# Performance work log

Measured on AMD Instinct MI355X. Metric: run time of the kernel, lower is better.

Reference implementation:

```python
import jax, jax.numpy as jnp
import numpy as np
import math

D, H, L, FF, V = 512, 8, 6, 2048, 512
DK = D // H
EPS = 1e-5


def _pos_encoding(seq_len, d_model):
    pos = np.arange(seq_len, dtype=np.float32)[:, None]
    div = np.exp(np.arange(0, d_model, 2, dtype=np.float32) * (-math.log(10000.0) / d_model))
    pe = np.zeros((seq_len, d_model), dtype=np.float32)
    pe[:, 0::2] = np.sin(pos * div)
    pe[:, 1::2] = np.cos(pos * div)
    return jnp.asarray(pe)


def _layernorm(x, g, b):
    mu = jnp.mean(x, axis=-1, keepdims=True)
    var = jnp.mean(jnp.square(x - mu), axis=-1, keepdims=True)
    return (x - mu) * jax.lax.rsqrt(var + EPS) * g + b


def setup_inputs() -> dict:
    key = jax.random.key(0)
    ks = jax.random.split(key, 16)
    B, S = 4, 1024
    inp = {
        'input_ids': jax.random.randint(ks[0], (B, S), 0, V, dtype=jnp.int64),
        'attention_mask': jnp.ones((B, S), dtype=jnp.int32),
        'emb': 0.02 * jax.random.normal(ks[1], (V, D), jnp.float32),
        # per-layer stacked params, torch Linear layout [out, in]
        'wq': 0.02 * jax.random.normal(ks[2], (L, D, D), jnp.float32),
        'bq': jnp.zeros((L, D), jnp.float32),
        'wk': 0.02 * jax.random.normal(ks[3], (L, D, D), jnp.float32),
        'bk': jnp.zeros((L, D), jnp.float32),
        'wv': 0.02 * jax.random.normal(ks[4], (L, D, D), jnp.float32),
        'bv': jnp.zeros((L, D), jnp.float32),
        'wo': 0.02 * jax.random.normal(ks[5], (L, D, D), jnp.float32),
        'bo': jnp.zeros((L, D), jnp.float32),
        'ln1_g': jnp.ones((L, D), jnp.float32),
        'ln1_b': jnp.zeros((L, D), jnp.float32),
        'w1': 0.02 * jax.random.normal(ks[6], (L, FF, D), jnp.float32),
        'b1': jnp.zeros((L, FF), jnp.float32),
        'w2': 0.02 * jax.random.normal(ks[7], (L, D, FF), jnp.float32),
        'b2': jnp.zeros((L, D), jnp.float32),
        'ln2_g': jnp.ones((L, D), jnp.float32),
        'ln2_b': jnp.zeros((L, D), jnp.float32),
        'lnf_g': jnp.ones((D,), jnp.float32),
        'lnf_b': jnp.zeros((D,), jnp.float32),
        'lm_w': 0.02 * jax.random.normal(ks[8], (V, D), jnp.float32),
    }
    return inp


def reference(input_ids, attention_mask, emb, wq, bq, wk, bk, wv, bv, wo, bo,
              ln1_g, ln1_b, w1, b1, w2, b2, ln2_g, ln2_b, lnf_g, lnf_b, lm_w):
    B, S = input_ids.shape
    x = emb[input_ids] * math.sqrt(D) + _pos_encoding(S, D)[None]  # [B,S,D]
    causal = jnp.tril(jnp.ones((S, S), jnp.float32))
    mask = causal[None, None] * attention_mask[:, None, None, :].astype(jnp.float32)  # [B,1,S,S]

    def step(h, p):
        (lwq, lbq, lwk, lbk, lwv, lbv, lwo, lbo, g1, be1, lw1, lb1, lw2, lb2, g2, be2) = p
        q = (jnp.einsum('bsd,ed->bse', h, lwq) + lbq).reshape(B, S, H, DK).transpose(0, 2, 1, 3)
        k = (jnp.einsum('bsd,ed->bse', h, lwk) + lbk).reshape(B, S, H, DK).transpose(0, 2, 1, 3)
        v = (jnp.einsum('bsd,ed->bse', h, lwv) + lbv).reshape(B, S, H, DK).transpose(0, 2, 1, 3)
        scores = jnp.einsum('bhqd,bhkd->bhqk', q, k) / math.sqrt(DK)
        scores = jnp.where(mask == 0, jnp.float32(-1e9), scores)
        attn = jax.nn.softmax(scores, axis=-1)
        o = jnp.einsum('bhqk,bhkd->bhqd', attn, v).transpose(0, 2, 1, 3).reshape(B, S, D)
        o = jnp.einsum('bsd,ed->bse', o, lwo) + lbo
        h = _layernorm(h + o, g1, be1)
        f = jax.nn.relu(jnp.einsum('bsd,fd->bsf', h, lw1) + lb1)
        f = jnp.einsum('bsf,df->bsd', f, lw2) + lb2
        h = _layernorm(h + f, g2, be2)
        return h, None

    x, _ = jax.lax.scan(step, x, (wq, bq, wk, bk, wv, bv, wo, bo,
                                  ln1_g, ln1_b, w1, b1, w2, b2, ln2_g, ln2_b))
    x = _layernorm(x, lnf_g, lnf_b)
    logits = jnp.einsum('bsd,vd->bsv', x, lm_w)  # [B,S,V]
    return logits
```

## Files before the change

### kernel.cpp

```cpp
#include <hip/hip_runtime.h>
#include <math.h>

#define D_MODEL 512
#define NHEAD   8
#define DKH     64
#define NLAYER  6
#define FFDIM   2048
#define VOCAB   512
#define BB      4
#define SS      1024
#define NROWS   4096

typedef unsigned short ushort_t;
typedef short short8 __attribute__((ext_vector_type(8)));
typedef float f32x4  __attribute__((ext_vector_type(4)));

__device__ __forceinline__ float bf2f(ushort_t u) {
    union { float f; unsigned int i; } x; x.i = ((unsigned int)u) << 16; return x.f;
}
__device__ __forceinline__ ushort_t f2bf(float f) {
    union { float f; unsigned int i; } x; x.f = f;
    unsigned int r = x.i + 0x7FFFu + ((x.i >> 16) & 1u);
    return (ushort_t)(r >> 16);
}
__device__ __forceinline__ void gload_lds16(const void* g, void* l) {
    __builtin_amdgcn_global_load_lds(
        (const __attribute__((address_space(1))) void*)g,
        (__attribute__((address_space(3))) void*)l, 16, 0, 0);
}
__device__ __forceinline__ void block_barrier() {
    __builtin_amdgcn_s_barrier();
    __builtin_amdgcn_sched_barrier(0);
}

__global__ __launch_bounds__(256) void cvt_all(
    const float* __restrict__ wq, const float* __restrict__ wk, const float* __restrict__ wv,
    const float* __restrict__ wo, const float* __restrict__ w1, const float* __restrict__ w2,
    const float* __restrict__ bq, const float* __restrict__ bk, const float* __restrict__ bv,
    ushort_t* __restrict__ wl, float* __restrict__ bqkv,
    const float* __restrict__ lmw, ushort_t* __restrict__ lmwb,
    const int* __restrict__ am, float* __restrict__ mbias)
{
    const int bidx = blockIdx.x;
    const int tt = threadIdx.x;
    if (bidx < 18432) {
        int idx = bidx * 256 + tt;
        int e = idx * 4;
        int l = e / 3145728;
        int off = e - l * 3145728;
        float4 v;
        if (off < 786432) {
            if (off < 262144)       v = *(const float4*)(wq + l * 262144 + off);
            else if (off < 524288)  v = *(const float4*)(wk + l * 262144 + (off - 262144));
            else                    v = *(const float4*)(wv + l * 262144 + (off - 524288));
        } else if (off < 1048576)   v = *(const float4*)(wo + l * 262144 + (off - 786432));
        else if (off < 2097152)     v = *(const float4*)(w1 + l * 1048576 + (off - 1048576));
        else                        v = *(const float4*)(w2 + l * 1048576 + (off - 2097152));
        union { ushort_t u[4]; uint2 q; } pk;
        pk.u[0] = f2bf(v.x); pk.u[1] = f2bf(v.y); pk.u[2] = f2bf(v.z); pk.u[3] = f2bf(v.w);
        *(uint2*)(wl + e) = pk.q;
        if (idx < 2304) {
            int b4 = idx * 4;
            int bl = b4 / 1536;
            int r  = b4 - bl * 1536;
            float4 bv4;
            if (r < 512)       bv4 = *(const float4*)(bq + bl * 512 + r);
            else if (r < 1024) bv4 = *(const float4*)(bk + bl * 512 + (r - 512));
            else               bv4 = *(const float4*)(bv + bl * 512 + (r - 1024));
            *(float4*)(bqkv + b4) = bv4;
        }
    } else if (bidx < 18688) {
        int e = ((bidx - 18432) * 256 + tt) * 4;
        float4 v = *(const float4*)(lmw + e);
        union { ushort_t u[4]; uint2 q; } pk;
        pk.u[0] = f2bf(v.x); pk.u[1] = f2bf(v.y); pk.u[2] = f2bf(v.z); pk.u[3] = f2bf(v.w);
        *(uint2*)(lmwb + e) = pk.q;
    } else {
#pragma unroll
        for (int i = 0; i < 16; ++i) {
            int j = i * 256 + tt;
            mbias[j] = am[j] ? 0.f : -1e9f;
        }
    }
}

__global__ __launch_bounds__(256) void cvt_layer(
    const float* __restrict__ wq, const float* __restrict__ wk, const float* __restrict__ wv,
    const float* __restrict__ wo, const float* __restrict__ w1, const float* __restrict__ w2,
    const float* __restrict__ bq, const float* __restrict__ bk, const float* __restrict__ bv,
    ushort_t* __restrict__ wl, float* __restrict__ bqkv)
{
    int idx = blockIdx.x * 256 + threadIdx.x;
    int e = idx * 4;
    float4 v;
    if (e < 786432) {
        if (e < 262144)       v = *(const float4*)(wq + e);
        else if (e < 524288)  v = *(const float4*)(wk + (e - 262144));
        else                  v = *(const float4*)(wv + (e - 524288));
    } else if (e < 1048576)   v = *(const float4*)(wo + (e - 786432));
    else if (e < 2097152)     v = *(const float4*)(w1 + (e - 1048576));
    else                      v = *(const float4*)(w2 + (e - 2097152));
    union { ushort_t u[4]; uint2 q; } pk;
    pk.u[0] = f2bf(v.x); pk.u[1] = f2bf(v.y); pk.u[2] = f2bf(v.z); pk.u[3] = f2bf(v.w);
    *(uint2*)(wl + e) = pk.q;
    if (idx < 384) {
        int b4 = idx * 4;
        float4 bv4;
        if (b4 < 512)       bv4 = *(const float4*)(bq + b4);
        else if (b4 < 1024) bv4 = *(const float4*)(bk + (b4 - 512));
        else                bv4 = *(const float4*)(bv + (b4 - 1024));
        *(float4*)(bqkv + b4) = bv4;
    }
}

__global__ __launch_bounds__(256) void cvt_simple(
    const float* __restrict__ src, ushort_t* __restrict__ dst)
{
    int e = (blockIdx.x * 256 + threadIdx.x) * 4;
    float4 v = *(const float4*)(src + e);
    union { ushort_t u[4]; uint2 q; } pk;
    pk.u[0] = f2bf(v.x); pk.u[1] = f2bf(v.y); pk.u[2] = f2bf(v.z); pk.u[3] = f2bf(v.w);
    *(uint2*)(dst + e) = pk.q;
}

__global__ __launch_bounds__(256) void maskbias_kernel(
    const int* __restrict__ am, float* __restrict__ mb)
{
    int i = blockIdx.x * 256 + threadIdx.x;
    if (i < NROWS) mb[i] = am[i] ? 0.f : -1e9f;
}

__global__ __launch_bounds__(512) void embed_kernel(
    const int* __restrict__ ids, const float* __restrict__ emb,
    float* __restrict__ xf, ushort_t* __restrict__ xb)
{
    int row = blockIdx.x;
    int d   = threadIdx.x;
    int s   = row & (SS - 1);
    int tok = ids[row];
    float div = expf(-(float)(d & ~1) * 0.0179889460390586f);
    float arg = (float)s * div;
    float pe  = (d & 1) ? cosf(arg) : sinf(arg);
    float v = emb[(size_t)tok * D_MODEL + d] * 22.62741699796952f + pe;
    xf[(size_t)row * D_MODEL + d] = v;
    xb[(size_t)row * D_MODEL + d] = f2bf(v);
}

__global__ __launch_bounds__(512) void ln_kernel(
    const float* __restrict__ x, const float* __restrict__ g,
    const float* __restrict__ b, float* __restrict__ outf, ushort_t* __restrict__ outb)
{
    int row = blockIdx.x;
    int d   = threadIdx.x;
    int wave = d >> 6, lane = d & 63;
    __shared__ float red[8];

    float v = x[(size_t)row * D_MODEL + d];
    float s = v;
#pragma unroll
    for (int o = 32; o > 0; o >>= 1) s += __shfl_xor(s, o);
    if (lane == 0) red[wave] = s;
    __syncthreads();
    float tot = 0.f;
#pragma unroll
    for (int i = 0; i < 8; ++i) tot += red[i];
    float mu = tot * (1.0f / D_MODEL);
    float c  = v - mu;
    __syncthreads();
    float s2 = c * c;
#pragma unroll
    for (int o = 32; o > 0; o >>= 1) s2 += __shfl_xor(s2, o);
    if (lane == 0) red[wave] = s2;
    __syncthreads();
    float tot2 = 0.f;
#pragma unroll
    for (int i = 0; i < 8; ++i) tot2 += red[i];
    float var = tot2 * (1.0f / D_MODEL);
    float y = c * (1.0f / sqrtf(var + 1e-5f)) * g[d] + b[d];
    outf[(size_t)row * D_MODEL + d] = y;
    outb[(size_t)row * D_MODEL + d] = f2bf(y);
}

template<int BM, int BN, bool RELU, bool RES, bool OBF16, bool VT>
__global__ __launch_bounds__(256) void gemm_kernel(
    const ushort_t* __restrict__ A, const ushort_t* __restrict__ W,
    const float* __restrict__ bias, const float* __restrict__ res,
    void* __restrict__ out, ushort_t* __restrict__ vtg, int M, int N, int K)
{
    constexpr int WMT = BM / 2, WNT = BN / 2;
    constexpr int FM = WMT / 16, FN = WNT / 16;
    constexpr int ISSA = BM / 32, ISSB = BN / 32;
    __shared__ ushort_t As[BM * 64];
    __shared__ ushort_t Bs[BN * 64];

    const int t = threadIdx.x;
    const int w = t >> 6, lane = t & 63;
    const int wr = w >> 1, wc = w & 1;
    const int col0 = blockIdx.x * BN;
    const int row0 = blockIdx.y * BM;
    const int lrow = lane & 15, kg = lane >> 4;
    const int srow = t >> 3;
    const int sk8  = (t & 7) ^ ((t >> 3) & 7);

    f32x4 acc[FM][FN];
#pragma unroll
    for (int m = 0; m < FM; ++m)
#pragma unroll
        for (int n = 0; n < FN; ++n) acc[m][n] = (f32x4){0.f, 0.f, 0.f, 0.f};

    for (int k0 = 0; k0 < K; k0 += 64) {
#pragma unroll
        for (int i = 0; i < ISSA; ++i)
            gload_lds16(A + (size_t)(row0 + i * 32 + srow) * K + k0 + sk8 * 8,
                        (char*)As + i * 4096 + t * 16);
#pragma unroll
        for (int i = 0; i < ISSB; ++i)
            gload_lds16(W + (size_t)(col0 + i * 32 + srow) * K + k0 + sk8 * 8,
                        (char*)Bs + i * 4096 + t * 16);
        __syncthreads();
#pragma unroll
        for (int kk = 0; kk < 2; ++kk) {
            short8 af[FM], bfv[FN];
#pragma unroll
            for (int m = 0; m < FM; ++m) {
                const int row = wr * WMT + m * 16 + lrow;
                af[m] = *(const short8*)&As[row * 64 + (((kk * 4 + kg) ^ (lrow & 7)) << 3)];
            }
#pragma unroll
            for (int n = 0; n < FN; ++n) {
                const int col = wc * WNT + n * 16 + lrow;
                bfv[n] = *(const short8*)&Bs[col * 64 + (((kk * 4 + kg) ^ (lrow & 7)) << 3)];
            }
#pragma unroll
            for (int m = 0; m < FM; ++m)
#pragma unroll
                for (int n = 0; n < FN; ++n)
                    acc[m][n] = __builtin_amdgcn_mfma_f32_16x16x32_bf16(
                        af[m], bfv[n], acc[m][n], 0, 0, 0);
        }
        __syncthreads();
    }

    const int lrow4 = (lane >> 4) * 4;
    const int lcol  = lane & 15;
#pragma unroll
    for (int m = 0; m < FM; ++m)
#pragma unroll
        for (int n = 0; n < FN; ++n) {
            const int col = col0 + wc * WNT + n * 16 + lcol;
            const float bv = bias ? bias[col] : 0.f;
            const int row_base = row0 + wr * WMT + m * 16 + lrow4;
            if (VT && col >= 1024) {
                const int vh = (col - 1024) >> 6;
                const int vd = (col - 1024) & 63;
                const int bq = row_base >> 10;
                const int s0 = row_base & 1023;
                union { ushort_t u[4]; uint2 q; } pk;
#pragma unroll
                for (int j = 0; j < 4; ++j) pk.u[j] = f2bf(acc[m][n][j] + bv);
                *(uint2*)(vtg + ((size_t)(bq * 8 + vh) * 64 + vd) * 1024 + s0) = pk.q;
            } else {
#pragma unroll
                for (int j = 0; j < 4; ++j) {
                    const int row = row_base + j;
                    float v = acc[m][n][j] + bv;
                    if (RES)  v += res[(size_t)row * N + col];
                    if (RELU) v = fmaxf(v, 0.f);
                    if (OBF16) ((ushort_t*)out)[(size_t)row * N + col] = f2bf(v);
                    else       ((float*)out)[(size_t)row * N + col] = v;
                }
            }
        }
}

__global__ __launch_bounds__(256) void attn_kernel(
    const ushort_t* __restrict__ qkv, const ushort_t* __restrict__ vtg,
    const float* __restrict__ mbias, ushort_t* __restrict__ o)
{
    __shared__ ushort_t Kl[3][64 * 64];
    __shared__ ushort_t Vl[3][64 * 64];

    const int t = threadIdx.x, w = t >> 6, l = t & 63;
    const int bid = blockIdx.x;
    const int qt = 15 - (bid >> 5);
    const int bh = bid & 31, b = bh >> 3, h = bh & 7;
    const int q0 = qt * 64;
    const int lg = l >> 4, lr = l & 15;
    const int qi = q0 + w * 16 + lr;

    const ushort_t* qrow = qkv + (size_t)(b * SS + qi) * 1536 + h * 64;
    const short8 qa0 = *(const short8*)(qrow + lg * 8);
    const short8 qa1 = *(const short8*)(qrow + 32 + lg * 8);

    float m_run = -1e30f, l_run = 0.f;
    f32x4 oacc[4];
#pragma unroll
    for (int nb = 0; nb < 4; ++nb) oacc[nb] = (f32x4){0.f, 0.f, 0.f, 0.f};

    const int krow = 32 * ((lr >> 1) & 1) + 8 * (lr >> 2) + (lr & 1);
    const ushort_t* qkvK = qkv + (size_t)(b * SS) * 1536 + 512 + h * 64;
    const ushort_t* vtgB = vtg + (size_t)bh * 64 * 1024;
    const float*    mb0  = mbias + b * SS + 8 * lg;

    const int sr0 = t >> 3, sc0 = t & 7;

    auto STAGE = [&](int buf, int kt) {
#pragma unroll
        for (int p = 0; p < 2; ++p) {
            const int row = p * 32 + sr0;
            const int ch  = sc0 ^ ((row >> 3) & 7);
            gload_lds16(qkvK + (size_t)(kt * 64 + row) * 1536 + ch * 8,
                        (char*)&Kl[buf][0] + (p * 256 + t) * 16);
        }
#pragma unroll
        for (int p = 0; p < 2; ++p) {
            const int row = p * 32 + sr0;
            const int ch  = sc0 ^ (row & 7);
            gload_lds16(vtgB + (size_t)row * 1024 + kt * 64 + ch * 8,
                        (char*)&Vl[buf][0] + (p * 256 + t) * 16);
        }
    };

    auto COMPUTE = [&](int buf, int kt) {
        const ushort_t* Kb = &Kl[buf][0];
        const ushort_t* Vb = &Vl[buf][0];
        short8 kf[8], vf[8];
#pragma unroll
        for (int nf = 0; nf < 4; ++nf) {
            const int row = 2 * nf + krow;
            const int sw  = (row >> 3) & 7;
            kf[2 * nf]     = *(const short8*)&Kb[row * 64 + ((lg ^ sw) << 3)];
            kf[2 * nf + 1] = *(const short8*)&Kb[row * 64 + (((4 + lg) ^ sw) << 3)];
        }
#pragma unroll
        for (int nb = 0; nb < 4; ++nb) {
            const int row = 16 * nb + lr;
            const int sw  = row & 7;
            vf[2 * nb]     = *(const short8*)&Vb[row * 64 + ((lg ^ sw) << 3)];
            vf[2 * nb + 1] = *(const short8*)&Vb[row * 64 + (((4 + lg) ^ sw) << 3)];
        }
        const float* mrow = mb0 + kt * 64;
        const float4 mA = *(const float4*)(mrow);
        const float4 mB = *(const float4*)(mrow + 4);
        const float4 mC = *(const float4*)(mrow + 32);
        const float4 mD = *(const float4*)(mrow + 36);
        f32x4 s[4];
#pragma unroll
        for (int nf = 0; nf < 4; ++nf) {
            f32x4 a = (f32x4){0.f, 0.f, 0.f, 0.f};
            a = __builtin_amdgcn_mfma_f32_16x16x32_bf16(kf[2 * nf],     qa0, a, 0, 0, 0);
            a = __builtin_amdgcn_mfma_f32_16x16x32_bf16(kf[2 * nf + 1], qa1, a, 0, 0, 0);
            s[nf] = a;
        }
        const bool diag = (kt == qt);
        const int kbase = kt * 64 + 8 * lg;
#pragma unroll
        for (int nf = 0; nf < 4; ++nf) {
#pragma unroll
            for (int r = 0; r < 4; ++r) {
                const int e = r & 1, oo = (r >> 1) & 1;
                const int idx = 2 * nf + e;
                const float bias = oo ? (idx < 4 ? ((const float*)&mC)[idx] : ((const float*)&mD)[idx - 4])
                                      : (idx < 4 ? ((const float*)&mA)[idx] : ((const float*)&mB)[idx - 4]);
                float sv = s[nf][r] * 0.125f + bias;
                if (diag && (kbase + idx + 32 * oo) > qi) sv = -1e9f;
                s[nf][r] = sv;
            }
        }
        float pm[4];
#pragma unroll
        for (int nf = 0; nf < 4; ++nf)
            pm[nf] = fmaxf(fmaxf(s[nf][0], s[nf][1]), fmaxf(s[nf][2], s[nf][3]));
        float mx = fmaxf(fmaxf(pm[0], pm[1]), fmaxf(pm[2], pm[3]));
        mx = fmaxf(mx, __shfl_xor(mx, 16));
        mx = fmaxf(mx, __shfl_xor(mx, 32));
        const float mnew = fmaxf(m_run, mx);
        const float rs   = __expf(m_run - mnew);
        m_run = mnew;
        float ps[4];
#pragma unroll
        for (int nf = 0; nf < 4; ++nf) {
#pragma unroll
            for (int r = 0; r < 4; ++r) s[nf][r] = __expf(s[nf][r] - mnew);
            ps[nf] = (s[nf][0] + s[nf][1]) + (s[nf][2] + s[nf][3]);
        }
        float tsum = (ps[0] + ps[1]) + (ps[2] + ps[3]);
        tsum += __shfl_xor(tsum, 16);
        tsum += __shfl_xor(tsum, 32);
        l_run = l_run * rs + tsum;
#pragma unroll
        for (int nb = 0; nb < 4; ++nb)
#pragma unroll
            for (int r = 0; r < 4; ++r) oacc[nb][r] *= rs;
        union { unsigned u[4]; short8 s8; } pa0u, pa1u;
#pragma unroll
        for (int nf = 0; nf < 4; ++nf) {
            pa0u.u[nf] = ((unsigned)f2bf(s[nf][1]) << 16) | (unsigned)f2bf(s[nf][0]);
            pa1u.u[nf] = ((unsigned)f2bf(s[nf][3]) << 16) | (unsigned)f2bf(s[nf][2]);
        }
#pragma unroll
        for (int nb = 0; nb < 4; ++nb) {
            oacc[nb] = __builtin_amdgcn_mfma_f32_16x16x32_bf16(vf[2 * nb],     pa0u.s8, oacc[nb], 0, 0, 0);
            oacc[nb] = __builtin_amdgcn_mfma_f32_16x16x32_bf16(vf[2 * nb + 1], pa1u.s8, oacc[nb], 0, 0, 0);
        }
    };

    STAGE(0, 0);
    if (qt >= 1) STAGE(1, 1);
    int buf = 0;
    for (int kt = 0; kt <= qt; ++kt) {
        if (kt + 2 <= qt) {
            int nxt = buf + 2; if (nxt >= 3) nxt -= 3;
            STAGE(nxt, kt + 2);
            asm volatile("s_waitcnt vmcnt(8)" ::: "memory");
        } else if (kt + 1 <= qt) {
            asm volatile("s_waitcnt vmcnt(4)" ::: "memory");
        } else {
            asm volatile("s_waitcnt vmcnt(0)" ::: "memory");
        }
        block_barrier();
        COMPUTE(buf, kt);
        block_barrier();
        if (++buf == 3) buf = 0;
    }

    const float inv = 1.0f / l_run;
    ushort_t* orow = o + (size_t)(b * SS + qi) * 512 + h * 64;
#pragma unroll
    for (int nb = 0; nb < 4; ++nb) {
        union { ushort_t u[4]; uint2 q; } pk;
#pragma unroll
        for (int r = 0; r < 4; ++r) pk.u[r] = f2bf(oacc[nb][r] * inv);
        *(uint2*)(orow + nb * 16 + 4 * lg) = pk.q;
    }
}

extern "C" void kernel_launch(void* const* d_in, const int* in_sizes, int n_in,
                              void* d_out, int out_size, void* d_ws, size_t ws_size,
                              hipStream_t stream)
{
    const int*   ids   = (const int*)d_in[0];
    const int*   am    = (const int*)d_in[1];
    const float* emb   = (const float*)d_in[2];
    const float* wq    = (const float*)d_in[3];
    const float* bq    = (const float*)d_in[4];
    const float* wk    = (const float*)d_in[5];
    const float* bk    = (const float*)d_in[6];
    const float* wv    = (const float*)d_in[7];
    const float* bv    = (const float*)d_in[8];
    const float* wo    = (const float*)d_in[9];
    const float* bo    = (const float*)d_in[10];
    const float* ln1g  = (const float*)d_in[11];
    const float* ln1b  = (const float*)d_in[12];
    const float* w1    = (const float*)d_in[13];
    const float* b1    = (const float*)d_in[14];
    const float* w2    = (const float*)d_in[15];
    const float* b2    = (const float*)d_in[16];
    const float* ln2g  = (const float*)d_in[17];
    const float* ln2b  = (const float*)d_in[18];
    const float* lnfg  = (const float*)d_in[19];
    const float* lnfb  = (const float*)d_in[20];
    const float* lmw   = (const float*)d_in[21];

    char* base = (char*)d_ws;
    float*    h    = (float*)(base);
    float*    h2   = (float*)(base + 8388608);
    ushort_t* hb   = (ushort_t*)(base + 16777216);
    ushort_t* act  = (ushort_t*)(base + 20971520);
    ushort_t* qkvb = act;
    ushort_t* ob   = act + 6291456;
    ushort_t* fbuf = act;
    ushort_t* vtg  = (ushort_t*)h2;

    const bool onep = ws_size >= (size_t)76100000;
    ushort_t* wl   = (ushort_t*)(base + 37748736);
    float*    bqkv; ushort_t* lmwb; float* mbias;
    if (onep) {
        bqkv  = (float*)(base + 75497472);
        lmwb  = (ushort_t*)(base + 75534336);
        mbias = (float*)(base + 76058624);
    } else {
        bqkv  = (float*)(base + 44040192);
        lmwb  = (ushort_t*)(base + 44046336);
        mbias = (float*)(base + 44570624);
    }

    embed_kernel<<<NROWS, 512, 0, stream>>>(ids, emb, h, hb);
    if (onep) {
        cvt_all<<<18689, 256, 0, stream>>>(wq, wk, wv, wo, w1, w2, bq, bk, bv,
                                           wl, bqkv, lmw, lmwb, am, mbias);
    } else {
        cvt_simple<<<256, 256, 0, stream>>>(lmw, lmwb);
        maskbias_kernel<<<16, 256, 0, stream>>>(am, mbias);
    }

    for (int l = 0; l < NLAYER; ++l) {
        const size_t dd = (size_t)l * 262144;
        const size_t fd = (size_t)l * 1048576;
        ushort_t* lw; const float* lb;
        if (onep) {
            lw = wl + (size_t)l * 3145728;
            lb = bqkv + l * 1536;
        } else {
            cvt_layer<<<3072, 256, 0, stream>>>(wq + dd, wk + dd, wv + dd, wo + dd,
                                                w1 + fd, w2 + fd,
                                                bq + l * 512, bk + l * 512, bv + l * 512,
                                                wl, bqkv);
            lw = wl;
            lb = bqkv;
        }
        gemm_kernel<64, 128, false, false, true, true><<<dim3(12, 64), 256, 0, stream>>>(
            hb, lw, lb, nullptr, qkvb, vtg, NROWS, 1536, 512);

        attn_kernel<<<512, 256, 0, stream>>>(qkvb, vtg, mbias, ob);

        gemm_kernel<64, 64, false, true, false, false><<<dim3(8, 64), 256, 0, stream>>>(
            ob, lw + 786432, bo + l * 512, h, h2, nullptr, NROWS, 512, 512);
        ln_kernel<<<NROWS, 512, 0, stream>>>(h2, ln1g + l * 512, ln1b + l * 512, h, hb);

        gemm_kernel<64, 128, true, false, true, false><<<dim3(16, 64), 256, 0, stream>>>(
            hb, lw + 1048576, b1 + l * 2048, nullptr, fbuf, nullptr, NROWS, 2048, 512);
        gemm_kernel<64, 64, false, true, false, false><<<dim3(8, 64), 256, 0, stream>>>(
            fbuf, lw + 2097152, b2 + l * 512, h, h2, nullptr, NROWS, 512, 2048);
        ln_kernel<<<NROWS, 512, 0, stream>>>(h2, ln2g + l * 512, ln2b + l * 512, h, hb);
    }

    ln_kernel<<<NROWS, 512, 0, stream>>>(h, lnfg, lnfb, h, hb);
    gemm_kernel<64, 64, false, false, false, false><<<dim3(8, 64), 256, 0, stream>>>(
        hb, lmwb, nullptr, nullptr, d_out, nullptr, NROWS, 512, 512);
}
```

Baseline: 704.8 us.

## Add multi-stage LDS prefetch pipeline with explicit vmcnt waits to GEMM

Adds a DEPTH template parameter to the GEMM so global-to-LDS loads for upcoming K tiles are issued before computing the current tile, with double or triple buffering chosen per call site. Synchronisation uses explicit s_waitcnt vmcnt counts plus raw barriers instead of __syncthreads. The goal is to overlap memory latency with MFMA work. In exchange it uses more shared memory, which may lower occupancy, and it relies on the vmcnt counts matching the number of loads each stage issues.

```diff
diff --git a/kernel.cpp b/kernel.cpp
--- a/kernel.cpp
+++ b/kernel.cpp
@@ -27,6 +27,13 @@
     __builtin_amdgcn_global_load_lds(
         (const __attribute__((address_space(1))) void*)g,
         (__attribute__((address_space(3))) void*)l, 16, 0, 0);
+}
+template<int N> __device__ __forceinline__ void waitcnt_vm() {
+    if constexpr (N == 0)      asm volatile("s_waitcnt vmcnt(0)" ::: "memory");
+    else if constexpr (N == 4) asm volatile("s_waitcnt vmcnt(4)" ::: "memory");
+    else if constexpr (N == 6) asm volatile("s_waitcnt vmcnt(6)" ::: "memory");
+    else if constexpr (N == 8) asm volatile("s_waitcnt vmcnt(8)" ::: "memory");
+    else if constexpr (N == 12) asm volatile("s_waitcnt vmcnt(12)" ::: "memory");
 }
 __device__ __forceinline__ void block_barrier() {
     __builtin_amdgcn_s_barrier();
@@ -181,7 +188,7 @@
     outb[(size_t)row * D_MODEL + d] = f2bf(y);
 }
 
-template<int BM, int BN, bool RELU, bool RES, bool OBF16, bool VT>
+template<int BM, int BN, int DEPTH, bool RELU, bool RES, bool OBF16, bool VT>
 __global__ __launch_bounds__(256) void gemm_kernel(
     const ushort_t* __restrict__ A, const ushort_t* __restrict__ W,
     const float* __restrict__ bias, const float* __restrict__ res,
@@ -190,8 +197,9 @@
     constexpr int WMT = BM / 2, WNT = BN / 2;
     constexpr int FM = WMT / 16, FN = WNT / 16;
     constexpr int ISSA = BM / 32, ISSB = BN / 32;
-    __shared__ ushort_t As[BM * 64];
-    __shared__ ushort_t Bs[BN * 64];
+    constexpr int NL = ISSA + ISSB;
+    __shared__ ushort_t As[DEPTH][BM * 64];
+    __shared__ ushort_t Bs[DEPTH][BN * 64];
 
     const int t = threadIdx.x;
     const int w = t >> 6, lane = t & 63;
@@ -208,28 +216,50 @@
 #pragma unroll
         for (int n = 0; n < FN; ++n) acc[m][n] = (f32x4){0.f, 0.f, 0.f, 0.f};
 
-    for (int k0 = 0; k0 < K; k0 += 64) {
+    auto STAGE = [&](int sb, int k0) {
 #pragma unroll
         for (int i = 0; i < ISSA; ++i)
             gload_lds16(A + (size_t)(row0 + i * 32 + srow) * K + k0 + sk8 * 8,
-                        (char*)As + i * 4096 + t * 16);
+                        (char*)&As[sb][0] + i * 4096 + t * 16);
 #pragma unroll
         for (int i = 0; i < ISSB; ++i)
             gload_lds16(W + (size_t)(col0 + i * 32 + srow) * K + k0 + sk8 * 8,
-                        (char*)Bs + i * 4096 + t * 16);
-        __syncthreads();
+                        (char*)&Bs[sb][0] + i * 4096 + t * 16);
+    };
+
+    const int NIT = K >> 6;
+    STAGE(0, 0);
+    if constexpr (DEPTH >= 3) { if (NIT > 1) STAGE(1, 64); }
+
+    int buf = 0;
+    for (int it = 0; it < NIT; ++it) {
+        if constexpr (DEPTH == 1) {
+            if (it > 0) STAGE(0, it * 64);
+            waitcnt_vm<0>();
+        } else if constexpr (DEPTH == 2) {
+            if (it + 1 < NIT) { STAGE(buf ^ 1, (it + 1) * 64); waitcnt_vm<NL>(); }
+            else              { waitcnt_vm<0>(); }
+        } else {
+            if (it + 2 < NIT) {
+                int nxt = buf + 2; if (nxt >= 3) nxt -= 3;
+                STAGE(nxt, (it + 2) * 64);
+                waitcnt_vm<2 * NL>();
+            } else if (it + 1 < NIT) { waitcnt_vm<NL>(); }
+            else                     { waitcnt_vm<0>(); }
+        }
+        block_barrier();
 #pragma unroll
         for (int kk = 0; kk < 2; ++kk) {
             short8 af[FM], bfv[FN];
 #pragma unroll
             for (int m = 0; m < FM; ++m) {
                 const int row = wr * WMT + m * 16 + lrow;
-                af[m] = *(const short8*)&As[row * 64 + (((kk * 4 + kg) ^ (lrow & 7)) << 3)];
+                af[m] = *(const short8*)&As[buf][row * 64 + (((kk * 4 + kg) ^ (lrow & 7)) << 3)];
             }
 #pragma unroll
             for (int n = 0; n < FN; ++n) {
                 const int col = wc * WNT + n * 16 + lrow;
-                bfv[n] = *(const short8*)&Bs[col * 64 + (((kk * 4 + kg) ^ (lrow & 7)) << 3)];
+                bfv[n] = *(const short8*)&Bs[buf][col * 64 + (((kk * 4 + kg) ^ (lrow & 7)) << 3)];
             }
 #pragma unroll
             for (int m = 0; m < FM; ++m)
@@ -238,7 +268,9 @@
                     acc[m][n] = __builtin_amdgcn_mfma_f32_16x16x32_bf16(
                         af[m], bfv[n], acc[m][n], 0, 0, 0);
         }
-        __syncthreads();
+        block_barrier();
+        if constexpr (DEPTH == 2) buf ^= 1;
+        else if constexpr (DEPTH == 3) { if (++buf == 3) buf = 0; }
     }
 
     const int lrow4 = (lane >> 4) * 4;
@@ -509,23 +541,23 @@
             lw = wl;
             lb = bqkv;
         }
-        gemm_kernel<64, 128, false, false, true, true><<<dim3(12, 64), 256, 0, stream>>>(
+        gemm_kernel<64, 128, 2, false, false, true, true><<<dim3(12, 64), 256, 0, stream>>>(
             hb, lw, lb, nullptr, qkvb, vtg, NROWS, 1536, 512);
 
         attn_kernel<<<512, 256, 0, stream>>>(qkvb, vtg, mbias, ob);
 
-        gemm_kernel<64, 64, false, true, false, false><<<dim3(8, 64), 256, 0, stream>>>(
+        gemm_kernel<64, 64, 3, false, true, false, false><<<dim3(8, 64), 256, 0, stream>>>(
             ob, lw + 786432, bo + l * 512, h, h2, nullptr, NROWS, 512, 512);
         ln_kernel<<<NROWS, 512, 0, stream>>>(h2, ln1g + l * 512, ln1b + l * 512, h, hb);
 
-        gemm_kernel<64, 128, true, false, true, false><<<dim3(16, 64), 256, 0, stream>>>(
+        gemm_kernel<64, 128, 1, true, false, true, false><<<dim3(16, 64), 256, 0, stream>>>(
             hb, lw + 1048576, b1 + l * 2048, nullptr, fbuf, nullptr, NROWS, 2048, 512);
-        gemm_kernel<64, 64, false, true, false, false><<<dim3(8, 64), 256, 0, stream>>>(
+        gemm_kernel<64, 64, 3, false, true, false, false><<<dim3(8, 64), 256, 0, stream>>>(
             fbuf, lw + 2097152, b2 + l * 512, h, h2, nullptr, NROWS, 512, 2048);
         ln_kernel<<<NROWS, 512, 0, stream>>>(h2, ln2g + l * 512, ln2b + l * 512, h, hb);
     }
 
     ln_kernel<<<NROWS, 512, 0, stream>>>(h, lnfg, lnfb, h, hb);
-    gemm_kernel<64, 64, false, false, false, false><<<dim3(8, 64), 256, 0, stream>>>(
+    gemm_kernel<64, 64, 3, false, false, false, false><<<dim3(8, 64), 256, 0, stream>>>(
         hb, lmwb, nullptr, nullptr, d_out, nullptr, NROWS, 512, 512);
 }
```

New measurement: 701.0 us. Within noise of the previous version (-0.5%).
